# Optimization experiments

Measured on AMD Instinct MI355X. Metric: run time of the kernel, lower is better.

The kernel has to match this reference:

```python
import jax, jax.numpy as jnp
import numpy as np

B, CH, H, W = 16, 4, 512, 512
HIDDEN = 8

def _filters():
    ident = jnp.array([[0.,0.,0.],[0.,1.,0.],[0.,0.,0.]])
    sobel_x = jnp.array([[-1.,0.,1.],[-2.,0.,2.],[-1.,0.,1.]])
    sobel_y = sobel_x.T
    lap = jnp.array([[1.,2.,1.],[2.,-12.,2.],[1.,2.,1.]])
    return jnp.stack([ident, sobel_x, sobel_y, lap])  # [4,3,3]

def setup_inputs() -> dict:
    key = jax.random.key(0)
    k1, k2, k3, k4, k5 = jax.random.split(key, 5)
    return {
        "x": jax.random.normal(k1, (B, CH, H, W), dtype=jnp.float32),
        "w1_w": jax.random.normal(k2, (HIDDEN, 4 * CH), dtype=jnp.float32) * 0.1,
        "w1_b": jax.random.normal(k3, (HIDDEN,), dtype=jnp.float32) * 0.1,
        "w2_w": jax.random.normal(k4, (CH, HIDDEN), dtype=jnp.float32) * 0.1,
        "noise": jax.random.uniform(k5, (B, 1, H, W), dtype=jnp.float32),
    }

def reference(x, w1_w, w1_b, w2_w, noise):
    filters = _filters()  # fixed (non-learned) perception kernels
    b, ch, h, w = x.shape
    # circular pad + per-channel (depthwise, 4 filters per channel) 3x3 conv
    xp = jnp.pad(x, ((0, 0), (0, 0), (1, 1), (1, 1)), mode="wrap")
    y = jax.lax.conv_general_dilated(
        xp.reshape(b * ch, 1, h + 2, w + 2),
        filters[:, None],  # [4,1,3,3]
        window_strides=(1, 1), padding="VALID",
        dimension_numbers=("NCHW", "OIHW", "NCHW"),
    ).reshape(b, ch * 4, h, w)  # channel order: (ch, filter)
    # 1x1 conv MLP: 16 -> 8 (relu) -> 4
    hdn = jax.nn.relu(jnp.einsum("bchw,oc->bohw", y, w1_w) + w1_b[None, :, None, None])
    dx = jnp.einsum("bchw,oc->bohw", hdn, w2_w)
    # stochastic update mask: floor(U[0,1) + update_rate), update_rate=0.5
    mask = jnp.floor(noise + 0.5)
    return x + dx * mask
```

## Files before the change

### kernel.cpp

```cpp
#include <hip/hip_runtime.h>
#include <math.h>

namespace {
typedef float v2f __attribute__((ext_vector_type(2)));

constexpr int B = 16, CH = 4, H = 512, W = 512, HID = 8;
constexpr int STRIP  = 8;
constexpr int SLOT_F = CH * W;
constexpr int NSLOT  = 5;

static __device__ __forceinline__ v2f splat(float f){ v2f r; r.x=f; r.y=f; return r; }

__global__ __launch_bounds__(256) void ca_kernel(
    const float* __restrict__ x,
    const float* __restrict__ w1w,
    const float* __restrict__ w1b,
    const float* __restrict__ w2w,
    const float* __restrict__ noise,
    float* __restrict__ out)
{
    __shared__ float smem[NSLOT * SLOT_F];

    const int blk  = blockIdx.x;
    const int b    = blk >> 6;
    const int hs   = (blk & 63) * STRIP;
    const int tid  = threadIdx.x;
    const int wv   = tid >> 6;
    const int lane = tid & 63;
    const int w0   = tid << 1;
    const int colL = (w0 - 1) & (W - 1);
    const int colR = (w0 + 2) & (W - 1);

    const float* xb = x + (size_t)b * CH * H * W;

    auto dma = [&](int q, int slot) {
        const int row  = q & (H - 1);
        const int half = wv & 1;
#pragma unroll
        for (int j = 0; j < 2; ++j) {
            const int ch = (wv >> 1) + 2 * j;
            const float* g = xb + ((size_t)ch * H + row) * W + half * 256 + lane * 4;
            const float* l = &smem[slot * SLOT_F + ch * W + half * 256];
            __builtin_amdgcn_global_load_lds(
                (const __attribute__((address_space(1))) void*)g,
                (__attribute__((address_space(3))) void*)l, 16, 0, 0);
        }
    };

    dma(hs - 1, 0); dma(hs, 1); dma(hs + 1, 2);
    asm volatile("" ::: "memory");
    dma(hs + 2, 3);

    int sA = 0, sB = 1, sC = 2, sW = 4;

    for (int i = 0; i < STRIP; ++i) {
        const int r = hs + i;
        if (i == 0)              asm volatile("s_waitcnt vmcnt(2)" ::: "memory");
        else if (i == STRIP - 1) asm volatile("s_waitcnt vmcnt(5)" ::: "memory");
        else                     asm volatile("s_waitcnt vmcnt(7)" ::: "memory");
        __builtin_amdgcn_s_barrier();
        if (i + 3 <= STRIP) dma(r + 3, sW);

        v2f hpre[HID];
#pragma unroll
        for (int o = 0; o < HID; ++o) hpre[o] = splat(w1b[o]);
        v2f xcv[CH];

#pragma unroll
        for (int ch = 0; ch < CH; ++ch) {
            const float* rT = &smem[sA * SLOT_F + ch * W];
            const float* rM = &smem[sB * SLOT_F + ch * W];
            const float* rB2 = &smem[sC * SLOT_F + ch * W];
            const float2 t2 = *(const float2*)&rT[w0];
            const float2 m2 = *(const float2*)&rM[w0];
            const float2 b2 = *(const float2*)&rB2[w0];
            const float tL = rT[colL], tR = rT[colR];
            const float mL = rM[colL], mR = rM[colR];
            const float bL = rB2[colL], bR = rB2[colR];

            v2f tv; tv.x = t2.x; tv.y = t2.y;
            v2f mv; mv.x = m2.x; mv.y = m2.y;
            v2f bv; bv.x = b2.x; bv.y = b2.y;
            const v2f sP = __builtin_elementwise_fma(splat(2.f), mv, tv + bv);
            const v2f dP = bv - tv;
            const float sL = fmaf(2.f, mL, tL + bL);
            const float sR = fmaf(2.f, mR, tR + bR);
            const float dL = bL - tL, dR = bR - tR;

            v2f sprev; sprev.x = sL;   sprev.y = sP.x;
            v2f snext; snext.x = sP.y; snext.y = sR;
            v2f dprev; dprev.x = dL;   dprev.y = dP.x;
            v2f dnext; dnext.x = dP.y; dnext.y = dR;

            const v2f id = mv;
            const v2f sx = snext - sprev;
            const v2f sy = __builtin_elementwise_fma(splat(2.f), dP, dprev + dnext);
            const v2f lp = __builtin_elementwise_fma(splat(-16.f), mv,
                            __builtin_elementwise_fma(splat(2.f), sP, sprev + snext));
            xcv[ch] = mv;
#pragma unroll
            for (int o = 0; o < HID; ++o) {
                const float* w1r = w1w + o * 16 + ch * 4;
                v2f a = hpre[o];
                a = __builtin_elementwise_fma(id, splat(w1r[0]), a);
                a = __builtin_elementwise_fma(sx, splat(w1r[1]), a);
                a = __builtin_elementwise_fma(sy, splat(w1r[2]), a);
                a = __builtin_elementwise_fma(lp, splat(w1r[3]), a);
                hpre[o] = a;
            }
        }

#pragma unroll
        for (int o = 0; o < HID; ++o)
            hpre[o] = __builtin_elementwise_max(hpre[o], splat(0.f));

        const float2 nz = *(const float2*)&noise[((size_t)b * H + r) * W + w0];
        v2f mk; mk.x = floorf(nz.x + 0.5f); mk.y = floorf(nz.y + 0.5f);

#pragma unroll
        for (int ch = 0; ch < CH; ++ch) {
            v2f dd = splat(0.f);
#pragma unroll
            for (int o = 0; o < HID; ++o)
                dd = __builtin_elementwise_fma(hpre[o], splat(w2w[ch * HID + o]), dd);
            const v2f ov = __builtin_elementwise_fma(dd, mk, xcv[ch]);
            float2 st; st.x = ov.x; st.y = ov.y;
            *(float2*)&out[((size_t)(b * CH + ch) * H + r) * W + w0] = st;
        }

        sA = sB; sB = sC;
        sC = (sC + 1 == NSLOT) ? 0 : sC + 1;
        sW = (sW + 1 == NSLOT) ? 0 : sW + 1;
    }
}
}

extern "C" void kernel_launch(void* const* d_in, const int* in_sizes, int n_in,
                              void* d_out, int out_size, void* d_ws, size_t ws_size,
                              hipStream_t stream) {
    const float* x     = (const float*)d_in[0];
    const float* w1w   = (const float*)d_in[1];
    const float* w1b   = (const float*)d_in[2];
    const float* w2w   = (const float*)d_in[3];
    const float* noise = (const float*)d_in[4];
    float* out = (float*)d_out;

    const int blocks = B * (H / STRIP);
    ca_kernel<<<blocks, 256, 0, stream>>>(x, w1w, w1b, w2w, noise, out);
}
```

Before: 35.75 us.

## Process two rows per step with 512-thread blocks and deeper LDS ring

Doubles the block to 512 threads so each step computes two output rows at once, with 16-row strips and an 8-slot LDS ring buffer for prefetched input rows. The loop is fully unrolled with hand-tuned vmcnt waits, and neighbor columns are read as aligned float2 loads instead of scalar loads. The goal is fewer barriers per row, deeper prefetch and better memory-latency hiding. The cost is larger LDS use per block (64KB), which reduces occupancy, and fragile hand-counted waitcnt values.

```diff
diff --git a/kernel.cpp b/kernel.cpp
--- a/kernel.cpp
+++ b/kernel.cpp
@@ -5,13 +5,13 @@
 typedef float v2f __attribute__((ext_vector_type(2)));
 
 constexpr int B = 16, CH = 4, H = 512, W = 512, HID = 8;
-constexpr int STRIP  = 8;
+constexpr int STRIP  = 16;
 constexpr int SLOT_F = CH * W;
-constexpr int NSLOT  = 5;
+constexpr int NSLOT  = 8;
 
 static __device__ __forceinline__ v2f splat(float f){ v2f r; r.x=f; r.y=f; return r; }
 
-__global__ __launch_bounds__(256) void ca_kernel(
+__global__ __launch_bounds__(512) void ca_kernel(
     const float* __restrict__ x,
     const float* __restrict__ w1w,
     const float* __restrict__ w1b,
@@ -22,44 +22,40 @@
     __shared__ float smem[NSLOT * SLOT_F];
 
     const int blk  = blockIdx.x;
-    const int b    = blk >> 6;
-    const int hs   = (blk & 63) * STRIP;
+    const int b    = blk >> 5;
+    const int hs   = (blk & 31) * STRIP;
     const int tid  = threadIdx.x;
     const int wv   = tid >> 6;
     const int lane = tid & 63;
-    const int w0   = tid << 1;
-    const int colL = (w0 - 1) & (W - 1);
-    const int colR = (w0 + 2) & (W - 1);
+    const int rsel = tid >> 8;
+    const int w0   = (tid & 255) << 1;
+    const int pl   = (w0 - 2) & (W - 1);
+    const int pr   = (w0 + 2) & (W - 1);
 
     const float* xb = x + (size_t)b * CH * H * W;
+    const int dch   = wv >> 1;
+    const int dhalf = wv & 1;
 
-    auto dma = [&](int q, int slot) {
+    auto dma = [&](int q) {
         const int row  = q & (H - 1);
-        const int half = wv & 1;
-#pragma unroll
-        for (int j = 0; j < 2; ++j) {
-            const int ch = (wv >> 1) + 2 * j;
-            const float* g = xb + ((size_t)ch * H + row) * W + half * 256 + lane * 4;
-            const float* l = &smem[slot * SLOT_F + ch * W + half * 256];
-            __builtin_amdgcn_global_load_lds(
-                (const __attribute__((address_space(1))) void*)g,
-                (__attribute__((address_space(3))) void*)l, 16, 0, 0);
-        }
+        const int slot = (q - hs + 1) & (NSLOT - 1);
+        const float* g = xb + ((size_t)dch * H + row) * W + dhalf * 256 + lane * 4;
+        const float* l = &smem[slot * SLOT_F + dch * W + dhalf * 256];
+        __builtin_amdgcn_global_load_lds(
+            (const __attribute__((address_space(1))) void*)g,
+            (__attribute__((address_space(3))) void*)l, 16, 0, 0);
     };
 
-    dma(hs - 1, 0); dma(hs, 1); dma(hs + 1, 2);
-    asm volatile("" ::: "memory");
-    dma(hs + 2, 3);
+    dma(hs - 1); dma(hs); dma(hs + 1); dma(hs + 2); dma(hs + 3); dma(hs + 4);
 
-    int sA = 0, sB = 1, sC = 2, sW = 4;
+    auto step = [&](int k) {
+        __builtin_amdgcn_s_barrier();
+        if (k <= 5) { dma(hs + 2 * k + 5); dma(hs + 2 * k + 6); }
 
-    for (int i = 0; i < STRIP; ++i) {
-        const int r = hs + i;
-        if (i == 0)              asm volatile("s_waitcnt vmcnt(2)" ::: "memory");
-        else if (i == STRIP - 1) asm volatile("s_waitcnt vmcnt(5)" ::: "memory");
-        else                     asm volatile("s_waitcnt vmcnt(7)" ::: "memory");
-        __builtin_amdgcn_s_barrier();
-        if (i + 3 <= STRIP) dma(r + 3, sW);
+        const int r  = hs + 2 * k + rsel;
+        const int sT = (2 * k + rsel)     & 7;
+        const int sM = (2 * k + rsel + 1) & 7;
+        const int sB = (2 * k + rsel + 2) & 7;
 
         v2f hpre[HID];
 #pragma unroll
@@ -68,24 +64,28 @@
 
 #pragma unroll
         for (int ch = 0; ch < CH; ++ch) {
-            const float* rT = &smem[sA * SLOT_F + ch * W];
-            const float* rM = &smem[sB * SLOT_F + ch * W];
-            const float* rB2 = &smem[sC * SLOT_F + ch * W];
-            const float2 t2 = *(const float2*)&rT[w0];
-            const float2 m2 = *(const float2*)&rM[w0];
-            const float2 b2 = *(const float2*)&rB2[w0];
-            const float tL = rT[colL], tR = rT[colR];
-            const float mL = rM[colL], mR = rM[colR];
-            const float bL = rB2[colL], bR = rB2[colR];
+            const float* T  = &smem[sT * SLOT_F + ch * W];
+            const float* M  = &smem[sM * SLOT_F + ch * W];
+            const float* Bt = &smem[sB * SLOT_F + ch * W];
+            const float2 t2 = *(const float2*)&T[w0];
+            const float2 tl = *(const float2*)&T[pl];
+            const float2 tr = *(const float2*)&T[pr];
+            const float2 m2 = *(const float2*)&M[w0];
+            const float2 ml = *(const float2*)&M[pl];
+            const float2 mr = *(const float2*)&M[pr];
+            const float2 b2 = *(const float2*)&Bt[w0];
+            const float2 bl = *(const float2*)&Bt[pl];
+            const float2 br = *(const float2*)&Bt[pr];
 
             v2f tv; tv.x = t2.x; tv.y = t2.y;
             v2f mv; mv.x = m2.x; mv.y = m2.y;
             v2f bv; bv.x = b2.x; bv.y = b2.y;
             const v2f sP = __builtin_elementwise_fma(splat(2.f), mv, tv + bv);
             const v2f dP = bv - tv;
-            const float sL = fmaf(2.f, mL, tL + bL);
-            const float sR = fmaf(2.f, mR, tR + bR);
-            const float dL = bL - tL, dR = bR - tR;
+            const float sL = fmaf(2.f, ml.y, tl.y + bl.y);
+            const float dL = bl.y - tl.y;
+            const float sR = fmaf(2.f, mr.x, tr.x + br.x);
+            const float dR = br.x - tr.x;
 
             v2f sprev; sprev.x = sL;   sprev.y = sP.x;
             v2f snext; snext.x = sP.y; snext.y = sR;
@@ -96,7 +96,7 @@
             const v2f sx = snext - sprev;
             const v2f sy = __builtin_elementwise_fma(splat(2.f), dP, dprev + dnext);
             const v2f lp = __builtin_elementwise_fma(splat(-16.f), mv,
-                            __builtin_elementwise_fma(splat(2.f), sP, sprev + snext));
+                             __builtin_elementwise_fma(splat(2.f), sP, sprev + snext));
             xcv[ch] = mv;
 #pragma unroll
             for (int o = 0; o < HID; ++o) {
@@ -127,11 +127,18 @@
             float2 st; st.x = ov.x; st.y = ov.y;
             *(float2*)&out[((size_t)(b * CH + ch) * H + r) * W + w0] = st;
         }
+    };
 
-        sA = sB; sB = sC;
-        sC = (sC + 1 == NSLOT) ? 0 : sC + 1;
-        sW = (sW + 1 == NSLOT) ? 0 : sW + 1;
-    }
+#define WAITVM(n) asm volatile("s_waitcnt vmcnt(" #n ")" ::: "memory")
+    WAITVM(2); step(0);
+    WAITVM(3); step(1);
+    WAITVM(4); step(2);
+    WAITVM(4); step(3);
+    WAITVM(4); step(4);
+    WAITVM(4); step(5);
+    WAITVM(4); step(6);
+    WAITVM(2); step(7);
+#undef WAITVM
 }
 }
 
@@ -146,5 +153,5 @@
     float* out = (float*)d_out;
 
     const int blocks = B * (H / STRIP);
-    ca_kernel<<<blocks, 256, 0, stream>>>(x, w1w, w1b, w2w, noise, out);
+    ca_kernel<<<blocks, 512, 0, stream>>>(x, w1w, w1b, w2w, noise, out);
 }
```

Result: faster. 34.96 us, median of 2 (-2.2%).

## Use one pixel per thread with 512 threads and prefetch noise row

Applied to the files above, without the earlier changes.

The block grows from 256 to 512 threads, and each thread now handles one column instead of two, so the packed v2f arithmetic becomes scalar. The DMA mapping changes to one global_load_lds per wave per row. Ring-slot indices are now computed from the loop counter, and the vmcnt wait thresholds are reworked. The noise value for the next row is prefetched one iteration ahead so its load overlaps the compute. This aims to raise occupancy and latency hiding, at the cost of losing the packed FMA throughput and doing more halo LDS reads per output.

```diff
diff --git a/kernel.cpp b/kernel.cpp
--- a/kernel.cpp
+++ b/kernel.cpp
@@ -2,16 +2,12 @@
 #include <math.h>
 
 namespace {
-typedef float v2f __attribute__((ext_vector_type(2)));
-
 constexpr int B = 16, CH = 4, H = 512, W = 512, HID = 8;
 constexpr int STRIP  = 8;
 constexpr int SLOT_F = CH * W;
 constexpr int NSLOT  = 5;
 
-static __device__ __forceinline__ v2f splat(float f){ v2f r; r.x=f; r.y=f; return r; }
-
-__global__ __launch_bounds__(256) void ca_kernel(
+__global__ __launch_bounds__(512) void ca_kernel(
     const float* __restrict__ x,
     const float* __restrict__ w1w,
     const float* __restrict__ w1b,
@@ -27,111 +23,97 @@
     const int tid  = threadIdx.x;
     const int wv   = tid >> 6;
     const int lane = tid & 63;
-    const int w0   = tid << 1;
-    const int colL = (w0 - 1) & (W - 1);
-    const int colR = (w0 + 2) & (W - 1);
+    const int cm   = (tid + W - 1) & (W - 1);
+    const int cp   = (tid + 1) & (W - 1);
 
     const float* xb = x + (size_t)b * CH * H * W;
+    const int dch   = wv >> 1;
+    const int dhalf = wv & 1;
 
-    auto dma = [&](int q, int slot) {
+    auto dma = [&](int q) {
         const int row  = q & (H - 1);
-        const int half = wv & 1;
+        const int slot = (q - hs + 1) % NSLOT;
+        const float* g = xb + ((size_t)dch * H + row) * W + dhalf * 256 + lane * 4;
+        const float* l = &smem[slot * SLOT_F + dch * W + dhalf * 256];
+        __builtin_amdgcn_global_load_lds(
+            (const __attribute__((address_space(1))) void*)g,
+            (__attribute__((address_space(3))) void*)l, 16, 0, 0);
+    };
+#define FENCE asm volatile("" ::: "memory")
+
+    dma(hs - 1); dma(hs); dma(hs + 1); FENCE;
+    dma(hs + 2); FENCE;
+    const float* nb = noise + (size_t)b * H * W;
+    float nz = nb[(size_t)hs * W + tid]; FENCE;
+
 #pragma unroll
-        for (int j = 0; j < 2; ++j) {
-            const int ch = (wv >> 1) + 2 * j;
-            const float* g = xb + ((size_t)ch * H + row) * W + half * 256 + lane * 4;
-            const float* l = &smem[slot * SLOT_F + ch * W + half * 256];
-            __builtin_amdgcn_global_load_lds(
-                (const __attribute__((address_space(1))) void*)g,
-                (__attribute__((address_space(3))) void*)l, 16, 0, 0);
-        }
-    };
+    for (int i = 0; i < STRIP; ++i) {
+        if      (i == 0) asm volatile("s_waitcnt vmcnt(2)"  ::: "memory");
+        else if (i == 1) asm volatile("s_waitcnt vmcnt(7)"  ::: "memory");
+        else if (i == 7) asm volatile("s_waitcnt vmcnt(10)" ::: "memory");
+        else             asm volatile("s_waitcnt vmcnt(11)" ::: "memory");
+        __builtin_amdgcn_s_barrier();
 
-    dma(hs - 1, 0); dma(hs, 1); dma(hs + 1, 2);
-    asm volatile("" ::: "memory");
-    dma(hs + 2, 3);
+        if (i <= 5) dma(hs + i + 3);
+        FENCE;
+        float nz_next = 0.f;
+        if (i <= 6) nz_next = nb[(size_t)((hs + i + 1) & (H - 1)) * W + tid];
+        FENCE;
 
-    int sA = 0, sB = 1, sC = 2, sW = 4;
+        const int r  = hs + i;
+        const int sT = i % NSLOT, sM = (i + 1) % NSLOT, sB = (i + 2) % NSLOT;
 
-    for (int i = 0; i < STRIP; ++i) {
-        const int r = hs + i;
-        if (i == 0)              asm volatile("s_waitcnt vmcnt(2)" ::: "memory");
-        else if (i == STRIP - 1) asm volatile("s_waitcnt vmcnt(5)" ::: "memory");
-        else                     asm volatile("s_waitcnt vmcnt(7)" ::: "memory");
-        __builtin_amdgcn_s_barrier();
-        if (i + 3 <= STRIP) dma(r + 3, sW);
-
-        v2f hpre[HID];
+        float hpre[HID];
 #pragma unroll
-        for (int o = 0; o < HID; ++o) hpre[o] = splat(w1b[o]);
-        v2f xcv[CH];
+        for (int o = 0; o < HID; ++o) hpre[o] = w1b[o];
+        float xc[CH];
 
 #pragma unroll
         for (int ch = 0; ch < CH; ++ch) {
-            const float* rT = &smem[sA * SLOT_F + ch * W];
-            const float* rM = &smem[sB * SLOT_F + ch * W];
-            const float* rB2 = &smem[sC * SLOT_F + ch * W];
-            const float2 t2 = *(const float2*)&rT[w0];
-            const float2 m2 = *(const float2*)&rM[w0];
-            const float2 b2 = *(const float2*)&rB2[w0];
-            const float tL = rT[colL], tR = rT[colR];
-            const float mL = rM[colL], mR = rM[colR];
-            const float bL = rB2[colL], bR = rB2[colR];
+            const float* T  = &smem[sT * SLOT_F + ch * W];
+            const float* M  = &smem[sM * SLOT_F + ch * W];
+            const float* Bt = &smem[sB * SLOT_F + ch * W];
+            const float tl = T[cm],  tc = T[tid],  tr = T[cp];
+            const float ml = M[cm],  mc = M[tid],  mr = M[cp];
+            const float bl = Bt[cm], bc = Bt[tid], br = Bt[cp];
 
-            v2f tv; tv.x = t2.x; tv.y = t2.y;
-            v2f mv; mv.x = m2.x; mv.y = m2.y;
-            v2f bv; bv.x = b2.x; bv.y = b2.y;
-            const v2f sP = __builtin_elementwise_fma(splat(2.f), mv, tv + bv);
-            const v2f dP = bv - tv;
-            const float sL = fmaf(2.f, mL, tL + bL);
-            const float sR = fmaf(2.f, mR, tR + bR);
-            const float dL = bL - tL, dR = bR - tR;
+            const float sl_ = fmaf(2.f, ml, tl + bl);
+            const float sc_ = fmaf(2.f, mc, tc + bc);
+            const float sr_ = fmaf(2.f, mr, tr + br);
+            const float dl_ = bl - tl, dc_ = bc - tc, dr_ = br - tr;
 
-            v2f sprev; sprev.x = sL;   sprev.y = sP.x;
-            v2f snext; snext.x = sP.y; snext.y = sR;
-            v2f dprev; dprev.x = dL;   dprev.y = dP.x;
-            v2f dnext; dnext.x = dP.y; dnext.y = dR;
-
-            const v2f id = mv;
-            const v2f sx = snext - sprev;
-            const v2f sy = __builtin_elementwise_fma(splat(2.f), dP, dprev + dnext);
-            const v2f lp = __builtin_elementwise_fma(splat(-16.f), mv,
-                            __builtin_elementwise_fma(splat(2.f), sP, sprev + snext));
-            xcv[ch] = mv;
+            const float id = mc;
+            const float sx = sr_ - sl_;
+            const float sy = fmaf(2.f, dc_, dl_ + dr_);
+            const float lp = fmaf(-16.f, mc, fmaf(2.f, sc_, sl_ + sr_));
+            xc[ch] = mc;
 #pragma unroll
             for (int o = 0; o < HID; ++o) {
                 const float* w1r = w1w + o * 16 + ch * 4;
-                v2f a = hpre[o];
-                a = __builtin_elementwise_fma(id, splat(w1r[0]), a);
-                a = __builtin_elementwise_fma(sx, splat(w1r[1]), a);
-                a = __builtin_elementwise_fma(sy, splat(w1r[2]), a);
-                a = __builtin_elementwise_fma(lp, splat(w1r[3]), a);
-                hpre[o] = a;
+                hpre[o] = fmaf(id, w1r[0],
+                          fmaf(sx, w1r[1],
+                          fmaf(sy, w1r[2],
+                          fmaf(lp, w1r[3], hpre[o]))));
             }
         }
 
 #pragma unroll
-        for (int o = 0; o < HID; ++o)
-            hpre[o] = __builtin_elementwise_max(hpre[o], splat(0.f));
+        for (int o = 0; o < HID; ++o) hpre[o] = fmaxf(hpre[o], 0.f);
 
-        const float2 nz = *(const float2*)&noise[((size_t)b * H + r) * W + w0];
-        v2f mk; mk.x = floorf(nz.x + 0.5f); mk.y = floorf(nz.y + 0.5f);
+        const float mk = floorf(nz + 0.5f);
 
 #pragma unroll
         for (int ch = 0; ch < CH; ++ch) {
-            v2f dd = splat(0.f);
+            float dd = 0.f;
 #pragma unroll
             for (int o = 0; o < HID; ++o)
-                dd = __builtin_elementwise_fma(hpre[o], splat(w2w[ch * HID + o]), dd);
-            const v2f ov = __builtin_elementwise_fma(dd, mk, xcv[ch]);
-            float2 st; st.x = ov.x; st.y = ov.y;
-            *(float2*)&out[((size_t)(b * CH + ch) * H + r) * W + w0] = st;
+                dd = fmaf(hpre[o], w2w[ch * HID + o], dd);
+            out[((size_t)(b * CH + ch) * H + r) * W + tid] = fmaf(dd, mk, xc[ch]);
         }
 
-        sA = sB; sB = sC;
-        sC = (sC + 1 == NSLOT) ? 0 : sC + 1;
-        sW = (sW + 1 == NSLOT) ? 0 : sW + 1;
+        nz = nz_next;
     }
+#undef FENCE
 }
 }
 
@@ -146,5 +128,5 @@
     float* out = (float*)d_out;
 
     const int blocks = B * (H / STRIP);
-    ca_kernel<<<blocks, 256, 0, stream>>>(x, w1w, w1b, w2w, noise, out);
+    ca_kernel<<<blocks, 512, 0, stream>>>(x, w1w, w1b, w2w, noise, out);
 }
```

New measurement: 37.66 us. 5.3% more time.
